# Performance work log

Measured on AMD Instinct MI355X. Metric: run time of the kernel, lower is better.

## Reference

```python
import jax, jax.numpy as jnp
import numpy as np

H = 256    # hidden_size
I = 512    # intermediate_size
S = 16     # ssm_state_size
R = 16     # time_step_rank = ceil(256/16)
K = 4      # conv_kernel
NL = 8     # num layers
EPS = 1e-5


def setup_inputs() -> dict:
    key = jax.random.key(0)
    ks = jax.random.split(key, 8)
    B, L = 16, 2048
    sc = 0.02
    x = jax.random.normal(ks[0], (B, L, H), jnp.float32)
    A_row = jnp.log(jnp.arange(1, S + 1, dtype=jnp.float32))  # HF init: A = 1..S
    return {
        "x": x,
        "norm_w": jnp.ones((NL, H), jnp.float32),
        "in_proj_w": jax.random.normal(ks[1], (NL, 2 * I, H), jnp.float32) * sc,
        "conv_w": jax.random.normal(ks[2], (NL, I, K), jnp.float32) * sc,
        "conv_b": jnp.zeros((NL, I), jnp.float32),
        "x_proj_w": jax.random.normal(ks[3], (NL, R + 2 * S, I), jnp.float32) * sc,
        "dt_proj_w": jax.random.normal(ks[4], (NL, I, R), jnp.float32) * sc,
        "dt_proj_b": jax.random.normal(ks[5], (NL, I), jnp.float32) * sc,
        "A_log": jnp.tile(A_row[None, None, :], (NL, I, 1)),
        "D": jnp.ones((NL, I), jnp.float32),
        "out_proj_w": jax.random.normal(ks[6], (NL, H, I), jnp.float32) * sc,
    }


def _rmsnorm(x, w):
    v = jnp.mean(x * x, axis=-1, keepdims=True)
    return x * jax.lax.rsqrt(v + EPS) * w


def _mamba_block(x, norm_w, in_w, cw, cb, xp_w, dt_w, dt_b, A_log, D_skip, out_w):
    B, L, _ = x.shape
    h = _rmsnorm(x, norm_w)
    proj = h @ in_w.T                               # (B, L, 2I)
    hs, gate = jnp.split(proj, 2, axis=-1)
    # depthwise causal conv over time
    hs_c = hs.transpose(0, 2, 1)                    # (B, I, L)
    conv = jax.lax.conv_general_dilated(
        hs_c, cw[:, None, :], window_strides=(1,), padding=[(K - 1, 0)],
        feature_group_count=I, dimension_numbers=("NCH", "OIH", "NCH"))
    u = jax.nn.silu(conv + cb[None, :, None]).transpose(0, 2, 1)  # (B, L, I)
    ssm_in = u @ xp_w.T                             # (B, L, R+2S)
    dt, Bm, Cm = jnp.split(ssm_in, [R, R + S], axis=-1)
    dt = jax.nn.softplus(dt @ dt_w.T + dt_b)        # (B, L, I)
    A = -jnp.exp(A_log)                             # (I, S)

    def step(state, inp):
        dt_t, B_t, C_t, u_t = inp                   # (B,I), (B,S), (B,S), (B,I)
        dA = jnp.exp(dt_t[:, :, None] * A)          # (B, I, S)
        state = dA * state + (dt_t * u_t)[:, :, None] * B_t[:, None, :]
        y = jnp.einsum("bis,bs->bi", state, C_t)
        return state, y

    init = jnp.zeros((B, I, S), x.dtype)
    xs = (dt.transpose(1, 0, 2), Bm.transpose(1, 0, 2),
          Cm.transpose(1, 0, 2), u.transpose(1, 0, 2))
    _, ys = jax.lax.scan(step, init, xs)            # (L, B, I)
    y = ys.transpose(1, 0, 2) + u * D_skip
    y = y * jax.nn.silu(gate)
    return x + y @ out_w.T


def reference(x, norm_w, in_proj_w, conv_w, conv_b, x_proj_w, dt_proj_w,
              dt_proj_b, A_log, D, out_proj_w):
    for li in range(NL):
        x = _mamba_block(x, norm_w[li], in_proj_w[li], conv_w[li], conv_b[li],
                         x_proj_w[li], dt_proj_w[li], dt_proj_b[li],
                         A_log[li], D[li], out_proj_w[li])
    return x
```

## Files before the change

### kernel.cpp

```cpp
#include <hip/hip_runtime.h>
#include <math.h>

#define HID 256
#define II 512
#define SS 16
#define RR 16
#define KC 4
#define NLAY 8
#define BATCH 16
#define LSEQ 2048
#define EPSV 1e-5f
#define NCCH 64
#define LCH (LSEQ/NCCH)
#define CSTR 130

typedef __attribute__((ext_vector_type(8))) short bf16x8;
typedef __attribute__((ext_vector_type(4))) float f32x4;
typedef __attribute__((ext_vector_type(2))) float f32x2;

#define GLOAD16(gp, lp) __builtin_amdgcn_global_load_lds( \
    (const __attribute__((address_space(1))) unsigned int*)(gp), \
    (__attribute__((address_space(3))) unsigned int*)(lp), 16, 0, 0)

__device__ __forceinline__ float silu_f(float x) { return x / (1.f + __expf(-x)); }
__device__ __forceinline__ float bf2f(unsigned short u) {
    union { unsigned int i; float f; } v; v.i = (unsigned int)u << 16; return v.f;
}
__device__ __forceinline__ unsigned short f2bf(float f) {
    union { float f; unsigned int i; } v; v.f = f;
    unsigned int r = v.i + 0x7FFFu + ((v.i >> 16) & 1u);
    return (unsigned short)(r >> 16);
}
__device__ __forceinline__ void powtree(float r, float* pw) {
    pw[0] = r; pw[1] = r * r; pw[3] = pw[1] * pw[1];
    pw[7] = pw[3] * pw[3]; pw[15] = pw[7] * pw[7];
    pw[2] = pw[1] * pw[0]; pw[4] = pw[3] * pw[0]; pw[5] = pw[3] * pw[1];
    pw[6] = pw[3] * pw[2]; pw[8] = pw[7] * pw[0]; pw[9] = pw[7] * pw[1];
    pw[10] = pw[7] * pw[2]; pw[11] = pw[7] * pw[3]; pw[12] = pw[7] * pw[4];
    pw[13] = pw[7] * pw[5]; pw[14] = pw[7] * pw[6];
}
__device__ __forceinline__ void powtree2(float r, f32x2* pw) {
    float r2 = r * r;
    float r4 = r2 * r2;
    float r8 = r4 * r4;
    pw[0] = (f32x2){r, r2};
    pw[1] = pw[0] * r2;
    pw[2] = pw[0] * r4;
    pw[3] = pw[1] * r4;
    pw[4] = pw[0] * r8;
    pw[5] = pw[1] * r8;
    pw[6] = pw[2] * r8;
    pw[7] = pw[3] * r8;
}

__global__ __launch_bounds__(256) void k_f2bf(const float* __restrict__ in,
                                              unsigned short* __restrict__ out, int n)
{
    for (int i = blockIdx.x * 256 + threadIdx.x; i < n; i += gridDim.x * 256)
        out[i] = f2bf(in[i]);
}

__global__ __launch_bounds__(256) void k_rmsnorm(const float* __restrict__ x,
                                                 const float* __restrict__ w,
                                                 unsigned short* __restrict__ out)
{
    int wave = threadIdx.x >> 6;
    int lane = threadIdx.x & 63;
    int row  = blockIdx.x * 4 + wave;
    const float* xr = x + (size_t)row * HID;
    float4 v = *(const float4*)(xr + lane * 4);
    float ss = v.x*v.x + v.y*v.y + v.z*v.z + v.w*v.w;
#pragma unroll
    for (int off = 32; off >= 1; off >>= 1) ss += __shfl_xor(ss, off, 64);
    float inv = 1.0f / sqrtf(ss * (1.0f / (float)HID) + EPSV);
    float4 wv = *(const float4*)(w + lane * 4);
    ushort4 o;
    o.x = f2bf(v.x * inv * wv.x); o.y = f2bf(v.y * inv * wv.y);
    o.z = f2bf(v.z * inv * wv.z); o.w = f2bf(v.w * inv * wv.w);
    *(ushort4*)(out + (size_t)row * HID + lane * 4) = o;
}

template<int RESID, int OUTBF>
__global__ __launch_bounds__(256) void k_gemm_mfma(const unsigned short* __restrict__ A,
                                                   const unsigned short* __restrict__ Bw,
                                                   const float* __restrict__ resid,
                                                   void* __restrict__ Cout,
                                                   int N, int K, int lda, int ntn)
{
    __shared__ unsigned short smem[16640];
    unsigned short* As = smem;
    unsigned short* Bs = smem + 8192;

    int ntm = gridDim.x / ntn;
    int mpx = ntm >> 3;
    int bid = blockIdx.x;
    int xcd = bid & 7, jj0 = bid >> 3;
    int mt = xcd * mpx + (jj0 % mpx);
    int nt = jj0 / mpx;
    int bm = mt * 128, bn = nt * 128;

    int tid = threadIdx.x;
    int wave = tid >> 6, lane = tid & 63;
    int wr = wave >> 1, wc = wave & 1;

    f32x4 acc[4][4];
#pragma unroll
    for (int mi = 0; mi < 4; mi++)
#pragma unroll
        for (int ni = 0; ni < 4; ni++) acc[mi][ni] = (f32x4){0.f, 0.f, 0.f, 0.f};

    int grp0 = wave * 4;
    int rr = lane >> 3, sl = lane & 7;
    int r = lane & 15, ks = lane >> 4;

    for (int k0 = 0; k0 < K; k0 += 64) {
        __syncthreads();
#pragma unroll
        for (int j = 0; j < 4; j++) {
            int g = grp0 + j;
            int row = g * 8 + rr;
            int ss = sl ^ (row & 7);
            GLOAD16(A + (size_t)(bm + row) * lda + k0 + ss * 8, As + g * 512);
            int br = bn + row; if (br > N - 1) br = N - 1;
            GLOAD16(Bw + (size_t)br * K + k0 + ss * 8, Bs + g * 512);
        }
        __syncthreads();
#pragma unroll
        for (int kk = 0; kk < 2; kk++) {
            bf16x8 af[4], bfv[4];
#pragma unroll
            for (int mi = 0; mi < 4; mi++) {
                int row = wr * 64 + mi * 16 + r;
                int boff = row * 128 + (((kk * 4 + ks) ^ (row & 7)) << 4);
                af[mi] = *(const bf16x8*)((const char*)As + boff);
            }
#pragma unroll
            for (int ni = 0; ni < 4; ni++) {
                int row = wc * 64 + ni * 16 + r;
                int boff = row * 128 + (((kk * 4 + ks) ^ (row & 7)) << 4);
                bfv[ni] = *(const bf16x8*)((const char*)Bs + boff);
            }
#pragma unroll
            for (int mi = 0; mi < 4; mi++)
#pragma unroll
                for (int ni = 0; ni < 4; ni++)
                    acc[mi][ni] = __builtin_amdgcn_mfma_f32_16x16x32_bf16(
                        af[mi], bfv[ni], acc[mi][ni], 0, 0, 0);
        }
    }

    int ccol = lane & 15, crow0 = (lane >> 4) * 4;
    if (OUTBF) {
        __syncthreads();
        unsigned short* Cs = smem;
#pragma unroll
        for (int mi = 0; mi < 4; mi++)
#pragma unroll
            for (int ni = 0; ni < 4; ni++) {
                int row = wr * 64 + mi * 16 + crow0;
                int col = wc * 64 + ni * 16 + ccol;
#pragma unroll
                for (int j = 0; j < 4; j++)
                    Cs[(row + j) * CSTR + col] = f2bf(acc[mi][ni][j]);
            }
        __syncthreads();
#pragma unroll
        for (int it = 0; it < 8; it++) {
            int idx = it * 256 + tid;
            int row = idx >> 4, ch = idx & 15;
            uint4 v = *(const uint4*)(Cs + row * CSTR + ch * 8);
            *(uint4*)((unsigned short*)Cout + (size_t)(bm + row) * N + bn + ch * 8) = v;
        }
    } else {
#pragma unroll
        for (int mi = 0; mi < 4; mi++)
#pragma unroll
            for (int ni = 0; ni < 4; ni++) {
                int gc = bn + wc * 64 + ni * 16 + ccol;
                if (gc < N) {
#pragma unroll
                    for (int j = 0; j < 4; j++) {
                        int gr = bm + wr * 64 + mi * 16 + crow0 + j;
                        float v = acc[mi][ni][j];
                        size_t off = (size_t)gr * N + gc;
                        if (RESID) v += resid[off];
                        ((float*)Cout)[off] = v;
                    }
                }
            }
    }
}

__global__ __launch_bounds__(256) void k_conv_silu(const unsigned short* __restrict__ proj,
                                                   const float* __restrict__ cw,
                                                   const float* __restrict__ cb,
                                                   unsigned short* __restrict__ u)
{
    __shared__ float sm[11][256];
    int tx = threadIdx.x;
    int t0 = blockIdx.x * 8;
    int i  = blockIdx.y * 256 + tx;
    int b  = blockIdx.z;
#pragma unroll
    for (int r = 0; r < 11; r++) {
        int t = t0 - 3 + r;
        float val = 0.f;
        if (t >= 0) val = bf2f(proj[(size_t)(b * LSEQ + t) * 1024 + i]);
        sm[r][tx] = val;
    }
    __syncthreads();
    float w0 = cw[i * KC + 0], w1 = cw[i * KC + 1], w2 = cw[i * KC + 2], w3 = cw[i * KC + 3];
    float bias = cb[i];
#pragma unroll
    for (int r = 0; r < 8; r++) {
        float s = sm[r][tx] * w0 + sm[r+1][tx] * w1 + sm[r+2][tx] * w2 + sm[r+3][tx] * w3 + bias;
        u[(size_t)(b * LSEQ + t0 + r) * II + i] = f2bf(silu_f(s));
    }
}

__device__ __forceinline__ bool a_is_integer(const float* alog, int i) {
    bool fast = true;
#pragma unroll
    for (int s = 0; s < SS; s++)
        fast = fast && (fabsf(expf(alog[i * SS + s]) - (float)(s + 1)) < 1e-3f);
    return fast;
}

__global__ __launch_bounds__(256) void k_scanA(const float* __restrict__ ssm,
                                               const unsigned short* __restrict__ u,
                                               const float* __restrict__ dtw,
                                               const float* __restrict__ dtb,
                                               const float* __restrict__ alog,
                                               float* __restrict__ P,
                                               float* __restrict__ S)
{
    __shared__ float sms[LCH][48];
    __shared__ unsigned short su[LCH][256];
    int tid = threadIdx.x;
    int i = blockIdx.x * 256 + tid;
    int c = blockIdx.y;
    int b = blockIdx.z;
    int t0c = c * LCH;
    size_t nbis = (size_t)gridDim.z * II * SS;

    const float* srb = ssm + ((size_t)b * LSEQ + t0c) * 48;
    for (int v = tid; v < LCH * 12; v += 256) {
        int t = v / 12, q = v - t * 12;
        *(float4*)&sms[t][q * 4] = *(const float4*)(srb + (size_t)t * 48 + q * 4);
    }
    const unsigned short* ubase = u + ((size_t)b * LSEQ + t0c) * II + (blockIdx.x << 8);
    for (int v = tid; v < LCH * 32; v += 256) {
        int t = v >> 5, c8 = (v & 31) << 3;
        *(uint4*)&su[t][c8] = *(const uint4*)(ubase + (size_t)t * II + c8);
    }
    __syncthreads();

    float bias = dtb[i];
    size_t o = (size_t)c * nbis + (((size_t)b * II + i) * SS);

    if (a_is_integer(alog, i)) {
        f32x2 wdt2[8];
#pragma unroll
        for (int k = 0; k < 8; k++) wdt2[k] = *(const f32x2*)(dtw + i * RR + k * 2);
        f32x2 Sr2[8];
#pragma unroll
        for (int k = 0; k < 8; k++) Sr2[k] = (f32x2){0.f, 0.f};
        float dtsum = 0.f;
        for (int t = 0; t < LCH; t++) {
            const f32x2* a2 = (const f32x2*)&sms[t][0];
            f32x2 d2 = (f32x2){bias, 0.f};
#pragma unroll
            for (int k = 0; k < 8; k++) d2 = __builtin_elementwise_fma(a2[k], wdt2[k], d2);
            float dacc = d2.x + d2.y;
            float e   = __expf(-fabsf(dacc));
            float dtv = fmaxf(dacc, 0.f) + __logf(1.f + e);
            float r   = __expf(-dtv);
            dtsum += dtv;
            float uv = bf2f(su[t][tid]);
            float du = dtv * uv;
            f32x2 du2 = (f32x2){du, du};
            f32x2 pw2[8]; powtree2(r, pw2);
            const f32x2* bv2 = (const f32x2*)&sms[t][16];
#pragma unroll
            for (int k = 0; k < 8; k++)
                Sr2[k] = __builtin_elementwise_fma(pw2[k], Sr2[k], du2 * bv2[k]);
        }
        f32x2 Pr2[8]; powtree2(__expf(-dtsum), Pr2);
#pragma unroll
        for (int k = 0; k < 8; k++) {
            *(f32x2*)(P + o + k * 2) = Pr2[k];
            *(f32x2*)(S + o + k * 2) = Sr2[k];
        }
    } else {
        float wdt[16];
#pragma unroll
        for (int q = 0; q < 4; q++) *(float4*)&wdt[q*4] = *(const float4*)(dtw + i * RR + q * 4);
        float Ac[SS];
#pragma unroll
        for (int s = 0; s < SS; s++) Ac[s] = -expf(alog[i * SS + s]);
        float Sr[SS], Pr[SS];
#pragma unroll
        for (int s = 0; s < SS; s++) { Sr[s] = 0.f; Pr[s] = 1.f; }
        for (int t = 0; t < LCH; t++) {
            float dacc = bias;
#pragma unroll
            for (int q = 0; q < 4; q++) {
                float4 a = *(const float4*)&sms[t][q * 4];
                dacc = fmaf(a.x, wdt[q*4+0], dacc); dacc = fmaf(a.y, wdt[q*4+1], dacc);
                dacc = fmaf(a.z, wdt[q*4+2], dacc); dacc = fmaf(a.w, wdt[q*4+3], dacc);
            }
            float e   = __expf(-fabsf(dacc));
            float dtv = fmaxf(dacc, 0.f) + __logf(1.f + e);
            float uv = bf2f(su[t][tid]);
            float du = dtv * uv;
#pragma unroll
            for (int q = 0; q < 4; q++) {
                float4 bv = *(const float4*)&sms[t][16 + q * 4];
                float dA0 = __expf(dtv * Ac[q*4+0]), dA1 = __expf(dtv * Ac[q*4+1]);
                float dA2 = __expf(dtv * Ac[q*4+2]), dA3 = __expf(dtv * Ac[q*4+3]);
                Pr[q*4+0] *= dA0; Pr[q*4+1] *= dA1; Pr[q*4+2] *= dA2; Pr[q*4+3] *= dA3;
                Sr[q*4+0] = fmaf(dA0, Sr[q*4+0], du * bv.x);
                Sr[q*4+1] = fmaf(dA1, Sr[q*4+1], du * bv.y);
                Sr[q*4+2] = fmaf(dA2, Sr[q*4+2], du * bv.z);
                Sr[q*4+3] = fmaf(dA3, Sr[q*4+3], du * bv.w);
            }
        }
#pragma unroll
        for (int q = 0; q < 4; q++) {
            *(float4*)(P + o + q*4) = make_float4(Pr[q*4], Pr[q*4+1], Pr[q*4+2], Pr[q*4+3]);
            *(float4*)(S + o + q*4) = make_float4(Sr[q*4], Sr[q*4+1], Sr[q*4+2], Sr[q*4+3]);
        }
    }
}

__global__ __launch_bounds__(256) void k_scanB(float* __restrict__ P,
                                               const float* __restrict__ S,
                                               int nbis)
{
    int idx = blockIdx.x * 256 + threadIdx.x;
    float carry = 0.f;
#pragma unroll 4
    for (int c = 0; c < NCCH - 1; c++) {
        size_t o = (size_t)c * nbis + idx;
        float Pv = P[o];
        float Sv = S[o];
        float nc = fmaf(Pv, carry, Sv);
        P[o] = carry;
        carry = nc;
    }
    P[(size_t)(NCCH - 1) * nbis + idx] = carry;
}

__global__ __launch_bounds__(256) void k_scanC(const float* __restrict__ ssm,
                                               const unsigned short* __restrict__ u,
                                               const float* __restrict__ dtw,
                                               const float* __restrict__ dtb,
                                               const float* __restrict__ alog,
                                               const float* __restrict__ st0,
                                               unsigned short* proj,
                                               const float* __restrict__ Dp)
{
    __shared__ float sms[LCH][48];
    __shared__ unsigned short su[LCH][256];
    int tid = threadIdx.x;
    int i = blockIdx.x * 256 + tid;
    int c = blockIdx.y;
    int b = blockIdx.z;
    int t0c = c * LCH;
    size_t nbis = (size_t)gridDim.z * II * SS;

    const float* srb = ssm + ((size_t)b * LSEQ + t0c) * 48;
    for (int v = tid; v < LCH * 12; v += 256) {
        int t = v / 12, q = v - t * 12;
        *(float4*)&sms[t][q * 4] = *(const float4*)(srb + (size_t)t * 48 + q * 4);
    }
    const unsigned short* ubase = u + ((size_t)b * LSEQ + t0c) * II + (blockIdx.x << 8);
    for (int v = tid; v < LCH * 32; v += 256) {
        int t = v >> 5, c8 = (v & 31) << 3;
        *(uint4*)&su[t][c8] = *(const uint4*)(ubase + (size_t)t * II + c8);
    }
    __syncthreads();

    float bias = dtb[i];
    float Dv = Dp[i];
    size_t o = (size_t)c * nbis + (((size_t)b * II + i) * SS);

    const unsigned short* gp = proj + ((size_t)b * LSEQ + t0c) * 1024 + 512 + i;
    unsigned short*       yp = proj + ((size_t)b * LSEQ + t0c) * 1024 + i;

    if (a_is_integer(alog, i)) {
        f32x2 wdt2[8];
#pragma unroll
        for (int k = 0; k < 8; k++) wdt2[k] = *(const f32x2*)(dtw + i * RR + k * 2);
        f32x2 st2[8];
#pragma unroll
        for (int k = 0; k < 8; k++) st2[k] = *(const f32x2*)(st0 + o + k * 2);
        for (int t = 0; t < LCH; t++) {
            const f32x2* a2 = (const f32x2*)&sms[t][0];
            f32x2 d2 = (f32x2){bias, 0.f};
#pragma unroll
            for (int k = 0; k < 8; k++) d2 = __builtin_elementwise_fma(a2[k], wdt2[k], d2);
            float dacc = d2.x + d2.y;
            float e   = __expf(-fabsf(dacc));
            float dtv = fmaxf(dacc, 0.f) + __logf(1.f + e);
            float r   = __expf(-dtv);
            float uv = bf2f(su[t][tid]);
            float du = dtv * uv;
            f32x2 du2 = (f32x2){du, du};
            f32x2 pw2[8]; powtree2(r, pw2);
            const f32x2* bv2 = (const f32x2*)&sms[t][16];
            const f32x2* cv2 = (const f32x2*)&sms[t][32];
            f32x2 acc2 = (f32x2){0.f, 0.f};
#pragma unroll
            for (int k = 0; k < 8; k++) {
                st2[k] = __builtin_elementwise_fma(pw2[k], st2[k], du2 * bv2[k]);
                acc2 = __builtin_elementwise_fma(st2[k], cv2[k], acc2);
            }
            float acc = acc2.x + acc2.y;
            float yv = acc + uv * Dv;
            float gv = bf2f(gp[(size_t)t * 1024]);
            yp[(size_t)t * 1024] = f2bf(yv * silu_f(gv));
        }
    } else {
        float wdt[16];
#pragma unroll
        for (int q = 0; q < 4; q++) *(float4*)&wdt[q*4] = *(const float4*)(dtw + i * RR + q * 4);
        float Ac[SS];
#pragma unroll
        for (int s = 0; s < SS; s++) Ac[s] = -expf(alog[i * SS + s]);
        float st[SS];
#pragma unroll
        for (int q = 0; q < 4; q++) *(float4*)&st[q*4] = *(const float4*)(st0 + o + q*4);
        for (int t = 0; t < LCH; t++) {
            float dacc = bias;
#pragma unroll
            for (int q = 0; q < 4; q++) {
                float4 a = *(const float4*)&sms[t][q * 4];
                dacc = fmaf(a.x, wdt[q*4+0], dacc); dacc = fmaf(a.y, wdt[q*4+1], dacc);
                dacc = fmaf(a.z, wdt[q*4+2], dacc); dacc = fmaf(a.w, wdt[q*4+3], dacc);
            }
            float e   = __expf(-fabsf(dacc));
            float dtv = fmaxf(dacc, 0.f) + __logf(1.f + e);
            float uv = bf2f(su[t][tid]);
            float du = dtv * uv;
            float acc = 0.f;
#pragma unroll
            for (int q = 0; q < 4; q++) {
                float4 bv = *(const float4*)&sms[t][16 + q * 4];
                float4 cv = *(const float4*)&sms[t][32 + q * 4];
                float dA0 = __expf(dtv * Ac[q*4+0]), dA1 = __expf(dtv * Ac[q*4+1]);
                float dA2 = __expf(dtv * Ac[q*4+2]), dA3 = __expf(dtv * Ac[q*4+3]);
                st[q*4+0] = fmaf(dA0, st[q*4+0], du * bv.x);
                st[q*4+1] = fmaf(dA1, st[q*4+1], du * bv.y);
                st[q*4+2] = fmaf(dA2, st[q*4+2], du * bv.z);
                st[q*4+3] = fmaf(dA3, st[q*4+3], du * bv.w);
                acc = fmaf(st[q*4+0], cv.x, acc); acc = fmaf(st[q*4+1], cv.y, acc);
                acc = fmaf(st[q*4+2], cv.z, acc); acc = fmaf(st[q*4+3], cv.w, acc);
            }
            float yv = acc + uv * Dv;
            float gv = bf2f(gp[(size_t)t * 1024]);
            yp[(size_t)t * 1024] = f2bf(yv * silu_f(gv));
        }
    }
}

extern "C" void kernel_launch(void* const* d_in, const int* in_sizes, int n_in,
                              void* d_out, int out_size, void* d_ws, size_t ws_size,
                              hipStream_t stream)
{
    const float* x_in   = (const float*)d_in[0];
    const float* norm_w = (const float*)d_in[1];
    const float* in_w   = (const float*)d_in[2];
    const float* conv_w = (const float*)d_in[3];
    const float* conv_b = (const float*)d_in[4];
    const float* xp_w   = (const float*)d_in[5];
    const float* dt_w   = (const float*)d_in[6];
    const float* dt_b   = (const float*)d_in[7];
    const float* alog   = (const float*)d_in[8];
    const float* Dp     = (const float*)d_in[9];
    const float* out_w  = (const float*)d_in[10];
    float* out = (float*)d_out;

    const size_t w_in  = (size_t)NLAY * 2 * II * HID;
    const size_t w_out = (size_t)NLAY * HID * II;
    const size_t w_xp  = (size_t)NLAY * 48 * II;
    const size_t wbytes = (w_in + w_out + w_xp) * 2;

    int Bc = 1;
    for (int cand = BATCH; cand >= 1; cand >>= 1) {
        size_t need = (size_t)cand * LSEQ * 1456 * sizeof(float) + wbytes + (1 << 20);
        if (need <= ws_size) { Bc = cand; break; }
    }
    size_t Mc = (size_t)Bc * LSEQ;
    int ntm = (int)(Mc / 128);
    int nbis = Bc * II * SS;

    float* wsf = (float*)d_ws;
    float*          ssm     = wsf;
    float*          P       = wsf + Mc * 48;
    float*          S       = wsf + Mc * 304;
    unsigned short* h_bf    = (unsigned short*)(wsf + Mc * 560);
    unsigned short* proj_bf = (unsigned short*)(wsf + Mc * 688);
    unsigned short* u_bf    = (unsigned short*)(wsf + Mc * 1200);
    unsigned short* inw_bf  = (unsigned short*)(wsf + Mc * 1456);
    unsigned short* outw_bf = inw_bf + w_in;
    unsigned short* xpw_bf  = outw_bf + w_out;

    k_f2bf<<<2048, 256, 0, stream>>>(in_w,  inw_bf,  (int)w_in);
    k_f2bf<<<2048, 256, 0, stream>>>(out_w, outw_bf, (int)w_out);
    k_f2bf<<<2048, 256, 0, stream>>>(xp_w,  xpw_bf,  (int)w_xp);

    const int nchunk = BATCH / Bc;

    for (int l = 0; l < NLAY; l++) {
        for (int c = 0; c < nchunk; c++) {
            size_t row0 = (size_t)c * Mc;
            const float* xsrc = (l == 0) ? x_in + row0 * HID : out + row0 * HID;
            float*       dst  = out + row0 * HID;

            k_rmsnorm<<<(int)(Mc / 4), 256, 0, stream>>>(xsrc, norm_w + l * HID, h_bf);
            k_gemm_mfma<0,1><<<ntm * 8, 256, 0, stream>>>(
                h_bf, inw_bf + (size_t)l * 2 * II * HID, nullptr, proj_bf,
                2 * II, HID, HID, 8);
            k_conv_silu<<<dim3(LSEQ / 8, 2, Bc), 256, 0, stream>>>(
                proj_bf, conv_w + (size_t)l * II * KC, conv_b + (size_t)l * II, u_bf);
            k_gemm_mfma<0,0><<<ntm, 256, 0, stream>>>(
                u_bf, xpw_bf + (size_t)l * 48 * II, nullptr, ssm, 48, II, II, 1);
            k_scanA<<<dim3(II / 256, NCCH - 1, Bc), 256, 0, stream>>>(
                ssm, u_bf, dt_w + (size_t)l * II * RR, dt_b + (size_t)l * II,
                alog + (size_t)l * II * SS, P, S);
            k_scanB<<<nbis / 256, 256, 0, stream>>>(P, S, nbis);
            k_scanC<<<dim3(II / 256, NCCH, Bc), 256, 0, stream>>>(
                ssm, u_bf, dt_w + (size_t)l * II * RR, dt_b + (size_t)l * II,
                alog + (size_t)l * II * SS, P, proj_bf, Dp + (size_t)l * II);
            k_gemm_mfma<1,0><<<ntm * 2, 256, 0, stream>>>(
                proj_bf, outw_bf + (size_t)l * HID * II, xsrc, dst, HID, II, 2 * II, 2);
        }
    }
}
```

Baseline: 2.009 ms.

## Process two interleaved sequence chunks per thread in scan kernels for ILP

k_scanA and k_scanC now have each thread handle two time chunks (c and c+32), interleaving the two independent recurrences so their dependency chains overlap. The grid's chunk dimension is halved. The u staging through shared memory is dropped in favour of direct per-thread global loads, and the slow non-integer-A path moves into helper functions. In exchange there are fewer blocks, higher register pressure, and uncoalesced-style strided global reads of u.

Result: no change. 1.980 ms (-1.5%).

```diff
diff --git a/kernel.cpp b/kernel.cpp
--- a/kernel.cpp
+++ b/kernel.cpp
@@ -31,14 +31,6 @@
     unsigned int r = v.i + 0x7FFFu + ((v.i >> 16) & 1u);
     return (unsigned short)(r >> 16);
 }
-__device__ __forceinline__ void powtree(float r, float* pw) {
-    pw[0] = r; pw[1] = r * r; pw[3] = pw[1] * pw[1];
-    pw[7] = pw[3] * pw[3]; pw[15] = pw[7] * pw[7];
-    pw[2] = pw[1] * pw[0]; pw[4] = pw[3] * pw[0]; pw[5] = pw[3] * pw[1];
-    pw[6] = pw[3] * pw[2]; pw[8] = pw[7] * pw[0]; pw[9] = pw[7] * pw[1];
-    pw[10] = pw[7] * pw[2]; pw[11] = pw[7] * pw[3]; pw[12] = pw[7] * pw[4];
-    pw[13] = pw[7] * pw[5]; pw[14] = pw[7] * pw[6];
-}
 __device__ __forceinline__ void powtree2(float r, f32x2* pw) {
     float r2 = r * r;
     float r4 = r2 * r2;
@@ -226,6 +218,75 @@
     return fast;
 }
 
+__device__ void scanA_slow_one(const float (*sm)[48], const unsigned short* up,
+                               const float* wdt, const float* Ac, float bias,
+                               float* Pr, float* Sr)
+{
+#pragma unroll
+    for (int s = 0; s < SS; s++) { Pr[s] = 1.f; Sr[s] = 0.f; }
+    for (int t = 0; t < LCH; t++) {
+        float dacc = bias;
+#pragma unroll
+        for (int q = 0; q < 4; q++) {
+            float4 a = *(const float4*)&sm[t][q * 4];
+            dacc = fmaf(a.x, wdt[q*4+0], dacc); dacc = fmaf(a.y, wdt[q*4+1], dacc);
+            dacc = fmaf(a.z, wdt[q*4+2], dacc); dacc = fmaf(a.w, wdt[q*4+3], dacc);
+        }
+        float e   = __expf(-fabsf(dacc));
+        float dtv = fmaxf(dacc, 0.f) + __logf(1.f + e);
+        float uv = bf2f(up[(size_t)t * II]);
+        float du = dtv * uv;
+#pragma unroll
+        for (int q = 0; q < 4; q++) {
+            float4 bv = *(const float4*)&sm[t][16 + q * 4];
+            float dA0 = __expf(dtv * Ac[q*4+0]), dA1 = __expf(dtv * Ac[q*4+1]);
+            float dA2 = __expf(dtv * Ac[q*4+2]), dA3 = __expf(dtv * Ac[q*4+3]);
+            Pr[q*4+0] *= dA0; Pr[q*4+1] *= dA1; Pr[q*4+2] *= dA2; Pr[q*4+3] *= dA3;
+            Sr[q*4+0] = fmaf(dA0, Sr[q*4+0], du * bv.x);
+            Sr[q*4+1] = fmaf(dA1, Sr[q*4+1], du * bv.y);
+            Sr[q*4+2] = fmaf(dA2, Sr[q*4+2], du * bv.z);
+            Sr[q*4+3] = fmaf(dA3, Sr[q*4+3], du * bv.w);
+        }
+    }
+}
+
+__device__ void scanC_slow_one(const float (*sm)[48], const unsigned short* up,
+                               const unsigned short* gp, unsigned short* yp,
+                               const float* wdt, const float* Ac, float bias,
+                               float Dv, float* st)
+{
+    for (int t = 0; t < LCH; t++) {
+        float dacc = bias;
+#pragma unroll
+        for (int q = 0; q < 4; q++) {
+            float4 a = *(const float4*)&sm[t][q * 4];
+            dacc = fmaf(a.x, wdt[q*4+0], dacc); dacc = fmaf(a.y, wdt[q*4+1], dacc);
+            dacc = fmaf(a.z, wdt[q*4+2], dacc); dacc = fmaf(a.w, wdt[q*4+3], dacc);
+        }
+        float e   = __expf(-fabsf(dacc));
+        float dtv = fmaxf(dacc, 0.f) + __logf(1.f + e);
+        float uv = bf2f(up[(size_t)t * II]);
+        float du = dtv * uv;
+        float acc = 0.f;
+#pragma unroll
+        for (int q = 0; q < 4; q++) {
+            float4 bv = *(const float4*)&sm[t][16 + q * 4];
+            float4 cv = *(const float4*)&sm[t][32 + q * 4];
+            float dA0 = __expf(dtv * Ac[q*4+0]), dA1 = __expf(dtv * Ac[q*4+1]);
+            float dA2 = __expf(dtv * Ac[q*4+2]), dA3 = __expf(dtv * Ac[q*4+3]);
+            st[q*4+0] = fmaf(dA0, st[q*4+0], du * bv.x);
+            st[q*4+1] = fmaf(dA1, st[q*4+1], du * bv.y);
+            st[q*4+2] = fmaf(dA2, st[q*4+2], du * bv.z);
+            st[q*4+3] = fmaf(dA3, st[q*4+3], du * bv.w);
+            acc = fmaf(st[q*4+0], cv.x, acc); acc = fmaf(st[q*4+1], cv.y, acc);
+            acc = fmaf(st[q*4+2], cv.z, acc); acc = fmaf(st[q*4+3], cv.w, acc);
+        }
+        float yv = acc + uv * Dv;
+        float gv = bf2f(gp[(size_t)t * 1024]);
+        yp[(size_t)t * 1024] = f2bf(yv * silu_f(gv));
+    }
+}
+
 __global__ __launch_bounds__(256) void k_scanA(const float* __restrict__ ssm,
                                                const unsigned short* __restrict__ u,
                                                const float* __restrict__ dtw,
@@ -234,62 +295,79 @@
                                                float* __restrict__ P,
                                                float* __restrict__ S)
 {
-    __shared__ float sms[LCH][48];
-    __shared__ unsigned short su[LCH][256];
+    __shared__ float sms[2][LCH][48];
     int tid = threadIdx.x;
     int i = blockIdx.x * 256 + tid;
     int c = blockIdx.y;
     int b = blockIdx.z;
-    int t0c = c * LCH;
+    int cB = c + 32;
+    bool twoOut = (cB < NCCH - 1);
     size_t nbis = (size_t)gridDim.z * II * SS;
 
-    const float* srb = ssm + ((size_t)b * LSEQ + t0c) * 48;
+    const float* srbA = ssm + ((size_t)b * LSEQ + c * LCH) * 48;
+    const float* srbB = ssm + ((size_t)b * LSEQ + cB * LCH) * 48;
     for (int v = tid; v < LCH * 12; v += 256) {
         int t = v / 12, q = v - t * 12;
-        *(float4*)&sms[t][q * 4] = *(const float4*)(srb + (size_t)t * 48 + q * 4);
-    }
-    const unsigned short* ubase = u + ((size_t)b * LSEQ + t0c) * II + (blockIdx.x << 8);
-    for (int v = tid; v < LCH * 32; v += 256) {
-        int t = v >> 5, c8 = (v & 31) << 3;
-        *(uint4*)&su[t][c8] = *(const uint4*)(ubase + (size_t)t * II + c8);
+        *(float4*)&sms[0][t][q * 4] = *(const float4*)(srbA + (size_t)t * 48 + q * 4);
+        *(float4*)&sms[1][t][q * 4] = *(const float4*)(srbB + (size_t)t * 48 + q * 4);
     }
     __syncthreads();
 
     float bias = dtb[i];
-    size_t o = (size_t)c * nbis + (((size_t)b * II + i) * SS);
+    const unsigned short* upA = u + ((size_t)b * LSEQ + c * LCH) * II + i;
+    const unsigned short* upB = u + ((size_t)b * LSEQ + cB * LCH) * II + i;
+    size_t oA = (size_t)c * nbis + (((size_t)b * II + i) * SS);
+    size_t oB = (size_t)cB * nbis + (((size_t)b * II + i) * SS);
 
     if (a_is_integer(alog, i)) {
         f32x2 wdt2[8];
 #pragma unroll
         for (int k = 0; k < 8; k++) wdt2[k] = *(const f32x2*)(dtw + i * RR + k * 2);
-        f32x2 Sr2[8];
-#pragma unroll
-        for (int k = 0; k < 8; k++) Sr2[k] = (f32x2){0.f, 0.f};
-        float dtsum = 0.f;
+        f32x2 SrA[8], SrB[8];
+#pragma unroll
+        for (int k = 0; k < 8; k++) { SrA[k] = (f32x2){0.f, 0.f}; SrB[k] = (f32x2){0.f, 0.f}; }
+        float dtsumA = 0.f, dtsumB = 0.f;
         for (int t = 0; t < LCH; t++) {
-            const f32x2* a2 = (const f32x2*)&sms[t][0];
-            f32x2 d2 = (f32x2){bias, 0.f};
-#pragma unroll
-            for (int k = 0; k < 8; k++) d2 = __builtin_elementwise_fma(a2[k], wdt2[k], d2);
-            float dacc = d2.x + d2.y;
-            float e   = __expf(-fabsf(dacc));
-            float dtv = fmaxf(dacc, 0.f) + __logf(1.f + e);
-            float r   = __expf(-dtv);
-            dtsum += dtv;
-            float uv = bf2f(su[t][tid]);
-            float du = dtv * uv;
-            f32x2 du2 = (f32x2){du, du};
-            f32x2 pw2[8]; powtree2(r, pw2);
-            const f32x2* bv2 = (const f32x2*)&sms[t][16];
-#pragma unroll
-            for (int k = 0; k < 8; k++)
-                Sr2[k] = __builtin_elementwise_fma(pw2[k], Sr2[k], du2 * bv2[k]);
-        }
-        f32x2 Pr2[8]; powtree2(__expf(-dtsum), Pr2);
+            const f32x2* aA = (const f32x2*)&sms[0][t][0];
+            const f32x2* aB = (const f32x2*)&sms[1][t][0];
+            f32x2 dA2 = (f32x2){bias, 0.f}, dB2 = (f32x2){bias, 0.f};
+#pragma unroll
+            for (int k = 0; k < 8; k++) {
+                dA2 = __builtin_elementwise_fma(aA[k], wdt2[k], dA2);
+                dB2 = __builtin_elementwise_fma(aB[k], wdt2[k], dB2);
+            }
+            float daccA = dA2.x + dA2.y, daccB = dB2.x + dB2.y;
+            float eA = __expf(-fabsf(daccA)), eB = __expf(-fabsf(daccB));
+            float dtA = fmaxf(daccA, 0.f) + __logf(1.f + eA);
+            float dtB = fmaxf(daccB, 0.f) + __logf(1.f + eB);
+            float rA = __expf(-dtA), rB = __expf(-dtB);
+            dtsumA += dtA; dtsumB += dtB;
+            float uvA = bf2f(upA[(size_t)t * II]), uvB = bf2f(upB[(size_t)t * II]);
+            float duA = dtA * uvA, duB = dtB * uvB;
+            f32x2 duA2 = (f32x2){duA, duA}, duB2 = (f32x2){duB, duB};
+            f32x2 pwA[8], pwB[8];
+            powtree2(rA, pwA); powtree2(rB, pwB);
+            const f32x2* bvA = (const f32x2*)&sms[0][t][16];
+            const f32x2* bvB = (const f32x2*)&sms[1][t][16];
+#pragma unroll
+            for (int k = 0; k < 8; k++) {
+                SrA[k] = __builtin_elementwise_fma(pwA[k], SrA[k], duA2 * bvA[k]);
+                SrB[k] = __builtin_elementwise_fma(pwB[k], SrB[k], duB2 * bvB[k]);
+            }
+        }
+        f32x2 PrA[8]; powtree2(__expf(-dtsumA), PrA);
 #pragma unroll
         for (int k = 0; k < 8; k++) {
-            *(f32x2*)(P + o + k * 2) = Pr2[k];
-            *(f32x2*)(S + o + k * 2) = Sr2[k];
+            *(f32x2*)(P + oA + k * 2) = PrA[k];
+            *(f32x2*)(S + oA + k * 2) = SrA[k];
+        }
+        if (twoOut) {
+            f32x2 PrB[8]; powtree2(__expf(-dtsumB), PrB);
+#pragma unroll
+            for (int k = 0; k < 8; k++) {
+                *(f32x2*)(P + oB + k * 2) = PrB[k];
+                *(f32x2*)(S + oB + k * 2) = SrB[k];
+            }
         }
     } else {
         float wdt[16];
@@ -298,37 +376,20 @@
         float Ac[SS];
 #pragma unroll
         for (int s = 0; s < SS; s++) Ac[s] = -expf(alog[i * SS + s]);
-        float Sr[SS], Pr[SS];
-#pragma unroll
-        for (int s = 0; s < SS; s++) { Sr[s] = 0.f; Pr[s] = 1.f; }
-        for (int t = 0; t < LCH; t++) {
-            float dacc = bias;
+        float Pr[SS], Sr[SS];
+        scanA_slow_one(sms[0], upA, wdt, Ac, bias, Pr, Sr);
+#pragma unroll
+        for (int q = 0; q < 4; q++) {
+            *(float4*)(P + oA + q*4) = make_float4(Pr[q*4], Pr[q*4+1], Pr[q*4+2], Pr[q*4+3]);
+            *(float4*)(S + oA + q*4) = make_float4(Sr[q*4], Sr[q*4+1], Sr[q*4+2], Sr[q*4+3]);
+        }
+        if (twoOut) {
+            scanA_slow_one(sms[1], upB, wdt, Ac, bias, Pr, Sr);
 #pragma unroll
             for (int q = 0; q < 4; q++) {
-                float4 a = *(const float4*)&sms[t][q * 4];
-                dacc = fmaf(a.x, wdt[q*4+0], dacc); dacc = fmaf(a.y, wdt[q*4+1], dacc);
-                dacc = fmaf(a.z, wdt[q*4+2], dacc); dacc = fmaf(a.w, wdt[q*4+3], dacc);
-            }
-            float e   = __expf(-fabsf(dacc));
-            float dtv = fmaxf(dacc, 0.f) + __logf(1.f + e);
-            float uv = bf2f(su[t][tid]);
-            float du = dtv * uv;
-#pragma unroll
-            for (int q = 0; q < 4; q++) {
-                float4 bv = *(const float4*)&sms[t][16 + q * 4];
-                float dA0 = __expf(dtv * Ac[q*4+0]), dA1 = __expf(dtv * Ac[q*4+1]);
-                float dA2 = __expf(dtv * Ac[q*4+2]), dA3 = __expf(dtv * Ac[q*4+3]);
-                Pr[q*4+0] *= dA0; Pr[q*4+1] *= dA1; Pr[q*4+2] *= dA2; Pr[q*4+3] *= dA3;
-                Sr[q*4+0] = fmaf(dA0, Sr[q*4+0], du * bv.x);
-                Sr[q*4+1] = fmaf(dA1, Sr[q*4+1], du * bv.y);
-                Sr[q*4+2] = fmaf(dA2, Sr[q*4+2], du * bv.z);
-                Sr[q*4+3] = fmaf(dA3, Sr[q*4+3], du * bv.w);
-            }
-        }
-#pragma unroll
-        for (int q = 0; q < 4; q++) {
-            *(float4*)(P + o + q*4) = make_float4(Pr[q*4], Pr[q*4+1], Pr[q*4+2], Pr[q*4+3]);
-            *(float4*)(S + o + q*4) = make_float4(Sr[q*4], Sr[q*4+1], Sr[q*4+2], Sr[q*4+3]);
+                *(float4*)(P + oB + q*4) = make_float4(Pr[q*4], Pr[q*4+1], Pr[q*4+2], Pr[q*4+3]);
+                *(float4*)(S + oB + q*4) = make_float4(Sr[q*4], Sr[q*4+1], Sr[q*4+2], Sr[q*4+3]);
+            }
         }
     }
 }
@@ -360,66 +421,82 @@
                                                unsigned short* proj,
                                                const float* __restrict__ Dp)
 {
-    __shared__ float sms[LCH][48];
-    __shared__ unsigned short su[LCH][256];
+    __shared__ float sms[2][LCH][48];
     int tid = threadIdx.x;
     int i = blockIdx.x * 256 + tid;
     int c = blockIdx.y;
     int b = blockIdx.z;
-    int t0c = c * LCH;
+    int cB = c + 32;
     size_t nbis = (size_t)gridDim.z * II * SS;
 
-    const float* srb = ssm + ((size_t)b * LSEQ + t0c) * 48;
+    const float* srbA = ssm + ((size_t)b * LSEQ + c * LCH) * 48;
+    const float* srbB = ssm + ((size_t)b * LSEQ + cB * LCH) * 48;
     for (int v = tid; v < LCH * 12; v += 256) {
         int t = v / 12, q = v - t * 12;
-        *(float4*)&sms[t][q * 4] = *(const float4*)(srb + (size_t)t * 48 + q * 4);
-    }
-    const unsigned short* ubase = u + ((size_t)b * LSEQ + t0c) * II + (blockIdx.x << 8);
-    for (int v = tid; v < LCH * 32; v += 256) {
-        int t = v >> 5, c8 = (v & 31) << 3;
-        *(uint4*)&su[t][c8] = *(const uint4*)(ubase + (size_t)t * II + c8);
+        *(float4*)&sms[0][t][q * 4] = *(const float4*)(srbA + (size_t)t * 48 + q * 4);
+        *(float4*)&sms[1][t][q * 4] = *(const float4*)(srbB + (size_t)t * 48 + q * 4);
     }
     __syncthreads();
 
     float bias = dtb[i];
     float Dv = Dp[i];
-    size_t o = (size_t)c * nbis + (((size_t)b * II + i) * SS);
-
-    const unsigned short* gp = proj + ((size_t)b * LSEQ + t0c) * 1024 + 512 + i;
-    unsigned short*       yp = proj + ((size_t)b * LSEQ + t0c) * 1024 + i;
+    size_t oA = (size_t)c * nbis + (((size_t)b * II + i) * SS);
+    size_t oB = (size_t)cB * nbis + (((size_t)b * II + i) * SS);
+
+    const unsigned short* upA = u + ((size_t)b * LSEQ + c * LCH) * II + i;
+    const unsigned short* upB = u + ((size_t)b * LSEQ + cB * LCH) * II + i;
+    const unsigned short* gpA = proj + ((size_t)b * LSEQ + c * LCH) * 1024 + 512 + i;
+    const unsigned short* gpB = proj + ((size_t)b * LSEQ + cB * LCH) * 1024 + 512 + i;
+    unsigned short* ypA = proj + ((size_t)b * LSEQ + c * LCH) * 1024 + i;
+    unsigned short* ypB = proj + ((size_t)b * LSEQ + cB * LCH) * 1024 + i;
 
     if (a_is_integer(alog, i)) {
         f32x2 wdt2[8];
 #pragma unroll
         for (int k = 0; k < 8; k++) wdt2[k] = *(const f32x2*)(dtw + i * RR + k * 2);
-        f32x2 st2[8];
-#pragma unroll
-        for (int k = 0; k < 8; k++) st2[k] = *(const f32x2*)(st0 + o + k * 2);
+        f32x2 stA[8], stB[8];
+#pragma unroll
+        for (int k = 0; k < 8; k++) {
+            stA[k] = *(const f32x2*)(st0 + oA + k * 2);
+            stB[k] = *(const f32x2*)(st0 + oB + k * 2);
+        }
         for (int t = 0; t < LCH; t++) {
-            const f32x2* a2 = (const f32x2*)&sms[t][0];
-            f32x2 d2 = (f32x2){bias, 0.f};
-#pragma unroll
-            for (int k = 0; k < 8; k++) d2 = __builtin_elementwise_fma(a2[k], wdt2[k], d2);
-            float dacc = d2.x + d2.y;
-            float e   = __expf(-fabsf(dacc));
-            float dtv = fmaxf(dacc, 0.f) + __logf(1.f + e);
-            float r   = __expf(-dtv);
-            float uv = bf2f(su[t][tid]);
-            float du = dtv * uv;
-            f32x2 du2 = (f32x2){du, du};
-            f32x2 pw2[8]; powtree2(r, pw2);
-            const f32x2* bv2 = (const f32x2*)&sms[t][16];
-            const f32x2* cv2 = (const f32x2*)&sms[t][32];
-            f32x2 acc2 = (f32x2){0.f, 0.f};
+            const f32x2* aA = (const f32x2*)&sms[0][t][0];
+            const f32x2* aB = (const f32x2*)&sms[1][t][0];
+            f32x2 dA2 = (f32x2){bias, 0.f}, dB2 = (f32x2){bias, 0.f};
 #pragma unroll
             for (int k = 0; k < 8; k++) {
-                st2[k] = __builtin_elementwise_fma(pw2[k], st2[k], du2 * bv2[k]);
-                acc2 = __builtin_elementwise_fma(st2[k], cv2[k], acc2);
-            }
-            float acc = acc2.x + acc2.y;
-            float yv = acc + uv * Dv;
-            float gv = bf2f(gp[(size_t)t * 1024]);
-            yp[(size_t)t * 1024] = f2bf(yv * silu_f(gv));
+                dA2 = __builtin_elementwise_fma(aA[k], wdt2[k], dA2);
+                dB2 = __builtin_elementwise_fma(aB[k], wdt2[k], dB2);
+            }
+            float daccA = dA2.x + dA2.y, daccB = dB2.x + dB2.y;
+            float eA = __expf(-fabsf(daccA)), eB = __expf(-fabsf(daccB));
+            float dtA = fmaxf(daccA, 0.f) + __logf(1.f + eA);
+            float dtB = fmaxf(daccB, 0.f) + __logf(1.f + eB);
+            float rA = __expf(-dtA), rB = __expf(-dtB);
+            float uvA = bf2f(upA[(size_t)t * II]), uvB = bf2f(upB[(size_t)t * II]);
+            float duA = dtA * uvA, duB = dtB * uvB;
+            f32x2 duA2 = (f32x2){duA, duA}, duB2 = (f32x2){duB, duB};
+            f32x2 pwA[8], pwB[8];
+            powtree2(rA, pwA); powtree2(rB, pwB);
+            const f32x2* bvA = (const f32x2*)&sms[0][t][16];
+            const f32x2* bvB = (const f32x2*)&sms[1][t][16];
+            const f32x2* cvA = (const f32x2*)&sms[0][t][32];
+            const f32x2* cvB = (const f32x2*)&sms[1][t][32];
+            f32x2 accA = (f32x2){0.f, 0.f}, accB = (f32x2){0.f, 0.f};
+#pragma unroll
+            for (int k = 0; k < 8; k++) {
+                stA[k] = __builtin_elementwise_fma(pwA[k], stA[k], duA2 * bvA[k]);
+                stB[k] = __builtin_elementwise_fma(pwB[k], stB[k], duB2 * bvB[k]);
+                accA = __builtin_elementwise_fma(stA[k], cvA[k], accA);
+                accB = __builtin_elementwise_fma(stB[k], cvB[k], accB);
+            }
+            float yvA = (accA.x + accA.y) + uvA * Dv;
+            float yvB = (accB.x + accB.y) + uvB * Dv;
+            float gvA = bf2f(gpA[(size_t)t * 1024]);
+            float gvB = bf2f(gpB[(size_t)t * 1024]);
+            ypA[(size_t)t * 1024] = f2bf(yvA * silu_f(gvA));
+            ypB[(size_t)t * 1024] = f2bf(yvB * silu_f(gvB));
         }
     } else {
         float wdt[16];
@@ -430,37 +507,11 @@
         for (int s = 0; s < SS; s++) Ac[s] = -expf(alog[i * SS + s]);
         float st[SS];
 #pragma unroll
-        for (int q = 0; q < 4; q++) *(float4*)&st[q*4] = *(const float4*)(st0 + o + q*4);
-        for (int t = 0; t < LCH; t++) {
-            float dacc = bias;
-#pragma unroll
-            for (int q = 0; q < 4; q++) {
-                float4 a = *(const float4*)&sms[t][q * 4];
-                dacc = fmaf(a.x, wdt[q*4+0], dacc); dacc = fmaf(a.y, wdt[q*4+1], dacc);
-                dacc = fmaf(a.z, wdt[q*4+2], dacc); dacc = fmaf(a.w, wdt[q*4+3], dacc);
-            }
-            float e   = __expf(-fabsf(dacc));
-            float dtv = fmaxf(dacc, 0.f) + __logf(1.f + e);
-            float uv = bf2f(su[t][tid]);
-            float du = dtv * uv;
-            float acc = 0.f;
-#pragma unroll
-            for (int q = 0; q < 4; q++) {
-                float4 bv = *(const float4*)&sms[t][16 + q * 4];
-                float4 cv = *(const float4*)&sms[t][32 + q * 4];
-                float dA0 = __expf(dtv * Ac[q*4+0]), dA1 = __expf(dtv * Ac[q*4+1]);
-                float dA2 = __expf(dtv * Ac[q*4+2]), dA3 = __expf(dtv * Ac[q*4+3]);
-                st[q*4+0] = fmaf(dA0, st[q*4+0], du * bv.x);
-                st[q*4+1] = fmaf(dA1, st[q*4+1], du * bv.y);
-                st[q*4+2] = fmaf(dA2, st[q*4+2], du * bv.z);
-                st[q*4+3] = fmaf(dA3, st[q*4+3], du * bv.w);
-                acc = fmaf(st[q*4+0], cv.x, acc); acc = fmaf(st[q*4+1], cv.y, acc);
-                acc = fmaf(st[q*4+2], cv.z, acc); acc = fmaf(st[q*4+3], cv.w, acc);
-            }
-            float yv = acc + uv * Dv;
-            float gv = bf2f(gp[(size_t)t * 1024]);
-            yp[(size_t)t * 1024] = f2bf(yv * silu_f(gv));
-        }
+        for (int q = 0; q < 4; q++) *(float4*)&st[q*4] = *(const float4*)(st0 + oA + q*4);
+        scanC_slow_one(sms[0], upA, gpA, ypA, wdt, Ac, bias, Dv, st);
+#pragma unroll
+        for (int q = 0; q < 4; q++) *(float4*)&st[q*4] = *(const float4*)(st0 + oB + q*4);
+        scanC_slow_one(sms[1], upB, gpB, ypB, wdt, Ac, bias, Dv, st);
     }
 }
 
@@ -526,11 +577,11 @@
                 proj_bf, conv_w + (size_t)l * II * KC, conv_b + (size_t)l * II, u_bf);
             k_gemm_mfma<0,0><<<ntm, 256, 0, stream>>>(
                 u_bf, xpw_bf + (size_t)l * 48 * II, nullptr, ssm, 48, II, II, 1);
-            k_scanA<<<dim3(II / 256, NCCH - 1, Bc), 256, 0, stream>>>(
+            k_scanA<<<dim3(II / 256, NCCH / 2, Bc), 256, 0, stream>>>(
                 ssm, u_bf, dt_w + (size_t)l * II * RR, dt_b + (size_t)l * II,
                 alog + (size_t)l * II * SS, P, S);
             k_scanB<<<nbis / 256, 256, 0, stream>>>(P, S, nbis);
-            k_scanC<<<dim3(II / 256, NCCH, Bc), 256, 0, stream>>>(
+            k_scanC<<<dim3(II / 256, NCCH / 2, Bc), 256, 0, stream>>>(
                 ssm, u_bf, dt_w + (size_t)l * II * RR, dt_b + (size_t)l * II,
                 alog + (size_t)l * II * SS, P, proj_bf, Dp + (size_t)l * II);
             k_gemm_mfma<1,0><<<ntm * 2, 256, 0, stream>>>(
```
